# Kernel tuning notes

Hardware: AMD Instinct MI355X
Metric: run time of the kernel (lower is better)

Reference implementation:

```python
import jax, jax.numpy as jnp
import numpy as np

N_DRUGS, N_TAILS, N_RELS = 10000, 20000, 100
E = 1_000_000
DIM = 64
SAMPLE_SIZE = 16
BN_EPS = 1e-5


def _xavier(k, shp):
    lim = np.sqrt(6.0 / (shp[0] + shp[1]))
    return jax.random.uniform(k, shp, jnp.float32, -lim, lim)


def setup_inputs() -> dict:
    key = jax.random.key(0)
    ks = jax.random.split(key, 12)
    DKG = jnp.stack([
        jax.random.randint(ks[0], (E,), 0, N_DRUGS, jnp.int32),   # head drug
        jax.random.randint(ks[1], (E,), 0, N_TAILS, jnp.int32),   # tail entity
        jax.random.randint(ks[2], (E,), 0, N_RELS, jnp.int32),    # relation
    ], axis=1)
    return {
        "HFEmbeding": jax.random.normal(ks[3], (N_DRUGS, DIM), jnp.float32),
        "X": jax.random.normal(ks[4], (N_DRUGS,), jnp.float32),
        "drug_emb": _xavier(ks[5], (N_DRUGS, DIM)),
        "rel_emb": _xavier(ks[6], (N_RELS, DIM)),
        "tail_emb": _xavier(ks[7], (N_TAILS, DIM)),
        "W1": _xavier(ks[8], (DIM, DIM)), "b1": jnp.zeros((DIM,), jnp.float32),
        "W2": _xavier(ks[9], (DIM, DIM)), "b2": jnp.zeros((DIM,), jnp.float32),
        "Wc": _xavier(ks[10], (2 * DIM, DIM)), "bc": jnp.zeros((DIM,), jnp.float32),
        "gamma": jnp.ones((DIM,), jnp.float32), "beta": jnp.zeros((DIM,), jnp.float32),
        "DKG": DKG,
    }


def _sampling_plan(head):
    """Vectorized stand-in for the per-node WeightedRandomSampler loop.
    deg >= S: uniform sample of S neighbor edges WITHOUT replacement (Gumbel-style
    per-segment random ranking). deg < S: keep all edges, plus (S - deg) extra
    draws WITH replacement. Purely index-valued; independent of float params."""
    k1, k2 = jax.random.split(jax.random.key(42))
    ones = jnp.ones_like(head)
    deg = jax.ops.segment_sum(ones, head, num_segments=N_DRUGS)          # [N]
    offsets = jnp.cumsum(deg) - deg                                      # CSR row starts
    r = jax.random.uniform(k1, head.shape)
    perm = jnp.lexsort((r, head))          # sorted by head, shuffled within segment
    head_sorted = head[perm]
    rank = jnp.arange(head.shape[0]) - offsets[head_sorted]
    keep = rank < SAMPLE_SIZE              # covers both branches' base sums
    # with-replacement extras for deg < S
    u = jax.random.randint(k2, (N_DRUGS, SAMPLE_SIZE), 0, jnp.iinfo(jnp.int32).max)
    safe_deg = jnp.maximum(deg, 1)
    extra_edge = perm[offsets[:, None] + u % safe_deg[:, None]]          # [N, S]
    need = jnp.clip(SAMPLE_SIZE - deg, 0)
    extra_mask = (jnp.arange(SAMPLE_SIZE)[None, :] < need[:, None]) & (deg[:, None] > 0)
    return perm, head_sorted, keep, extra_edge, extra_mask


def reference(HFEmbeding, X, drug_emb, rel_emb, tail_emb, W1, b1, W2, b2, Wc, bc, gamma, beta, DKG):
    head, tail, rel = DKG[:, 0], DKG[:, 1], DKG[:, 2]
    # edge semantics score: MLP(sigma) over hadamard of head & relation embeddings
    h = drug_emb[head] * rel_emb[rel]                       # [E, D]
    h = jax.nn.sigmoid(h @ W1 + b1) @ W2 + b2
    score = jnp.sum(h, axis=1, keepdims=True)               # [E, 1]
    temp = score * tail_emb[tail]                           # [E, D]
    perm, head_sorted, keep, extra_edge, extra_mask = _sampling_plan(head)
    neigh = jax.ops.segment_sum(jnp.where(keep[:, None], temp[perm], 0.0),
                                head_sorted, num_segments=N_DRUGS)       # [N, D]
    neigh = neigh + jnp.sum(temp[extra_edge] * extra_mask[..., None], axis=1)
    cat = jnp.concatenate([drug_emb, neigh], axis=1)        # [N, 2D]
    y = cat @ Wc + bc
    # BatchNorm1d, training mode (batch statistics, biased variance)
    mean = jnp.mean(y, axis=0)
    var = jnp.var(y, axis=0)
    out = gamma * (y - mean) * jax.lax.rsqrt(var + BN_EPS) + beta
    return (HFEmbeding, out, X)
```

## Files before the change

### kernel.cpp

```cpp
#include <hip/hip_runtime.h>
#include <stdint.h>

#define NDRUGS 10000
#define NTAILS 20000
#define NE     1000000
#define SSIZE  16
#define NPART  192
#define CSLOT  96

typedef unsigned int  u32;
typedef unsigned short u16;
typedef unsigned long long u64;
typedef __attribute__((ext_vector_type(8))) short bf16x8;
typedef __attribute__((ext_vector_type(4))) float f32x4;
#define U64MAX 0xffffffffffffffffULL

__host__ __device__ __forceinline__ void tf2x32(u32 k0, u32 k1, u32 x0, u32 x1,
                                                u32& o0, u32& o1) {
  u32 ks2 = k0 ^ k1 ^ 0x1BD11BDAu;
  x0 += k0; x1 += k1;
#define TFR(r) { x0 += x1; x1 = (x1 << r) | (x1 >> (32 - r)); x1 ^= x0; }
  TFR(13) TFR(15) TFR(26) TFR(6)
  x0 += k1; x1 += ks2 + 1u;
  TFR(17) TFR(29) TFR(16) TFR(24)
  x0 += ks2; x1 += k0 + 2u;
  TFR(13) TFR(15) TFR(26) TFR(6)
  x0 += k0; x1 += k1 + 3u;
  TFR(17) TFR(29) TFR(16) TFR(24)
  x0 += k1; x1 += ks2 + 4u;
  TFR(13) TFR(15) TFR(26) TFR(6)
  x0 += ks2; x1 += k0 + 5u;
#undef TFR
  o0 = x0; o1 = x1;
}

__device__ __forceinline__ u32 rbits32(u32 kx, u32 ky, u32 i) {
  u32 o0, o1;
  tf2x32(kx, ky, 0u, i, o0, o1);
  return o0 ^ o1;
}
#define SELKEY(e) ((((u64)(rbits32(k1x, k1y, (u32)(e)) >> 9)) << 32) | (u32)(e))
#define CSWAP(x, y) { u64 lo_ = x < y ? x : y; u64 hi_ = x < y ? y : x; x = lo_; y = hi_; }

__device__ __forceinline__ float q16(float f) {
  u32 x = __builtin_bit_cast(u32, f);
  u32 lsb = (x >> 16) & 1u;
  x = (x + 0x7fffu + lsb) & 0xffff0000u;
  return __builtin_bit_cast(float, x);
}
__device__ __forceinline__ u16 rne16(float f) {
  u32 x = __builtin_bit_cast(u32, f);
  u32 lsb = (x >> 16) & 1u;
  return (u16)((x + 0x7fffu + lsb) >> 16);
}
__device__ __forceinline__ float bfbits2f(u16 b) {
  u32 x = ((u32)b) << 16;
  return __builtin_bit_cast(float, x);
}

__global__ __launch_bounds__(256) void k_hist(const int4* __restrict__ dkg4,
                                              u32* __restrict__ part32) {
  __shared__ int hist[NDRUGS];
  for (int j = threadIdx.x; j < NDRUGS; j += 256) hist[j] = 0;
  __syncthreads();
  for (int i = blockIdx.x * 256 + threadIdx.x; i < NE / 4; i += NPART * 256) {
    int4 A = dkg4[3 * i], B = dkg4[3 * i + 1], C = dkg4[3 * i + 2];
    atomicAdd(&hist[A.x], 1);
    atomicAdd(&hist[A.w], 1);
    atomicAdd(&hist[B.z], 1);
    atomicAdd(&hist[C.y], 1);
  }
  __syncthreads();
  u32* p = part32 + blockIdx.x * (NDRUGS / 2);
  for (int j = threadIdx.x; j < NDRUGS / 2; j += 256)
    p[j] = (u32)hist[2 * j] | ((u32)hist[2 * j + 1] << 16);
}

__global__ __launch_bounds__(256) void k_thr(const u32* __restrict__ part32,
                                             int* __restrict__ deg,
                                             u32* __restrict__ thr,
                                             int* __restrict__ cnt,
                                             int* __restrict__ nflag) {
  int t = blockIdx.x * 256 + threadIdx.x;
  if (t == 0) *nflag = 0;
  if (t >= NDRUGS / 2) return;
  int d0 = 0, d1 = 0;
  for (int b = 0; b < NPART; b++) {
    u32 v = part32[b * (NDRUGS / 2) + t];
    d0 += (int)(v & 0xffffu);
    d1 += (int)(v >> 16);
  }
  int d = 2 * t;
  deg[d] = d0;  deg[d + 1] = d1;
  cnt[d] = 0;   cnt[d + 1] = 0;
  thr[d]     = (d0 <= 40) ? 0x800000u
                          : (402653184u + (u32)d0 - 1u) / (u32)d0;
  thr[d + 1] = (d1 <= 40) ? 0x800000u
                          : (402653184u + (u32)d1 - 1u) / (u32)d1;
}

__global__ __launch_bounds__(256) void k_cand(const int4* __restrict__ dkg4,
                                              const u32* __restrict__ thr,
                                              int* __restrict__ cnt,
                                              int* __restrict__ cand,
                                              int* __restrict__ nflag,
                                              int* __restrict__ flaglist,
                                              u32 k1x, u32 k1y) {
  __shared__ u32 thr_l[NDRUGS];
  for (int j = threadIdx.x; j < NDRUGS; j += 256) thr_l[j] = thr[j];
  __syncthreads();
  int i = blockIdx.x * 256 + threadIdx.x;
  if (i >= NE / 4) return;
  int4 A = dkg4[3 * i], B = dkg4[3 * i + 1], C = dkg4[3 * i + 2];
  int h[4] = {A.x, A.w, B.z, C.y};
  int e0 = 4 * i;
#pragma unroll
  for (int k = 0; k < 4; k++) {
    u32 rb = rbits32(k1x, k1y, (u32)(e0 + k));
    if ((rb >> 9) < thr_l[h[k]]) {
      int pos = atomicAdd(&cnt[h[k]], 1);
      if (pos < CSLOT) cand[h[k] * CSLOT + pos] = e0 + k;
      else if (pos == CSLOT) {
        int ix = atomicAdd(nflag, 1);
        if (ix < 256) flaglist[ix] = h[k];
      }
    }
  }
}

__global__ __launch_bounds__(256) void k_select(const int* __restrict__ cand,
                                                const int* __restrict__ cnt,
                                                const int* __restrict__ deg,
                                                int* __restrict__ sel,
                                                int* __restrict__ nflag,
                                                int* __restrict__ flaglist,
                                                u32 k1x, u32 k1y,
                                                u32 khx, u32 khy,
                                                u32 klx, u32 kly) {
  __shared__ int asel[4][16];
  int tid = threadIdx.x, lane = tid & 63, wv = tid >> 6;
  int d = blockIdx.x * 4 + wv;
  if (d >= NDRUGS) return;
  int dg = deg[d], n = cnt[d], off = d * CSLOT;
  if (dg <= 0) {
    if (lane < 16) sel[d * SSIZE + lane] = -1;
    return;
  }
  if (dg >= SSIZE) {
    if (n < SSIZE || n > CSLOT) {
      if (lane == 0) {
        int ix = atomicAdd(nflag, 1);
        if (ix < 256) flaglist[ix] = d;
      }
      return;
    }
    u64 a0 = U64MAX, a1 = U64MAX;
    if (lane < n)      a0 = SELKEY(cand[off + lane]);
    if (lane + 64 < n) a1 = SELKEY(cand[off + lane + 64]);
    CSWAP(a0, a1)
    int h = 0; u32 my = 0;
#pragma unroll
    for (int r = 0; r < SSIZE; r++) {
      u64 ex = (h == 0) ? a0 : (h == 1) ? a1 : U64MAX;
      u64 g = ex;
#pragma unroll
      for (int m = 1; m < 64; m <<= 1) {
        u64 o = __shfl_xor(g, m, 64);
        g = o < g ? o : g;
      }
      if (lane == r) my = (u32)g;
      if (ex == g) h++;
    }
    if (lane < 16) sel[d * SSIZE + lane] = (int)my;
  } else {
    u64 a0 = (lane < n) ? SELKEY(cand[off + lane]) : U64MAX;
    int h = 0;
    for (int r = 0; r < n; r++) {
      u64 ex = (h == 0) ? a0 : U64MAX;
      u64 g = ex;
#pragma unroll
      for (int m = 1; m < 64; m <<= 1) {
        u64 o = __shfl_xor(g, m, 64);
        g = o < g ? o : g;
      }
      if (lane == 0) asel[wv][r] = (int)(u32)g;
      if (ex == g) h++;
    }
    if (lane < n) sel[d * SSIZE + lane] = asel[wv][lane];
    int need = SSIZE - n;
    const u32 span = 0x7fffffffu;
    if (lane < need) {
      u32 j = (u32)(d * SSIZE + lane);
      u32 hi = rbits32(khx, khy, j) % span;
      u32 lo = rbits32(klx, kly, j) % span;
      u32 u = (hi * 2u + lo) % span;
      int idx = (int)(u % (u32)n);
      sel[d * SSIZE + n + lane] = asel[wv][idx];
    }
  }
}

__global__ __launch_bounds__(256) void k_fix(const int* __restrict__ dkg,
                                             const int* __restrict__ nflag,
                                             const int* __restrict__ flaglist,
                                             int* __restrict__ sel,
                                             u32 k1x, u32 k1y) {
  int nf = *nflag;
  if (nf <= 0) return;
  if (nf > 256) nf = 256;
  __shared__ u64 pool[256 * 16];
  int tid = threadIdx.x;
  for (int f = 0; f < nf; f++) {
    int d = flaglist[f];
    u64 loc[16];
#pragma unroll
    for (int i = 0; i < 16; i++) loc[i] = U64MAX;
    u64 mx = U64MAX; int mi = 0;
    for (int e = tid; e < NE; e += 256) {
      if (dkg[3 * e] == d) {
        u64 k = SELKEY(e);
        if (k < mx) {
          loc[mi] = k; mx = 0;
          for (int i = 0; i < 16; i++)
            if (loc[i] > mx) { mx = loc[i]; mi = i; }
        }
      }
    }
#pragma unroll
    for (int i = 0; i < 16; i++) pool[tid * 16 + i] = loc[i];
    __syncthreads();
    if (tid == 0) {
      u64 best[16];
#pragma unroll
      for (int i = 0; i < 16; i++) best[i] = U64MAX;
      u64 bm = U64MAX; int bi = 0;
      for (int i = 0; i < 256 * 16; i++) {
        u64 k = pool[i];
        if (k < bm) {
          best[bi] = k; bm = 0;
          for (int j = 0; j < 16; j++)
            if (best[j] > bm) { bm = best[j]; bi = j; }
        }
      }
      for (int s = 0; s < 16; s++) sel[d * SSIZE + s] = (int)(u32)best[s];
    }
    __syncthreads();
  }
}

__global__ __launch_bounds__(256, 2) void k_gather(const int* __restrict__ sel,
                                                   const int* __restrict__ dkg,
                                                   const float* __restrict__ drug,
                                                   const float* __restrict__ rel,
                                                   const float* __restrict__ tail,
                                                   const float* __restrict__ W1,
                                                   const float* __restrict__ b1,
                                                   const float* __restrict__ W2,
                                                   const float* __restrict__ b2,
                                                   float* __restrict__ neigh,
                                                   float* __restrict__ psq) {
  __shared__ __align__(16) u16 Vh[4][16][72];
  __shared__ __align__(16) u16 Vl[4][16][72];
  __shared__ float rsp[4][64];
  int tid = threadIdx.x, lane = tid & 63, wv = tid >> 6;
  int quad = lane >> 4, c = lane & 15;

  if (blockIdx.x == 0 && tid < 128) psq[tid] = 0.f;
  {
    int r_ = tid & 63, ks = tid >> 6;
    float s = 0.f;
    for (int k = ks * 16; k < ks * 16 + 16; k++) s += q16(W2[r_ * 64 + k]);
    rsp[ks][r_] = s;
  }
  __syncthreads();

  bf16x8 bw[4][2];
#pragma unroll
  for (int t = 0; t < 4; t++)
#pragma unroll
    for (int s = 0; s < 2; s++) {
      union { short h[8]; bf16x8 v; } u;
#pragma unroll
      for (int jj = 0; jj < 8; jj++)
        u.h[jj] = (short)rne16(W1[(s * 32 + quad * 8 + jj) * 64 + t * 16 + c]);
      bw[t][s] = u.v;
    }
  float b1t[4], w2t[4];
#pragma unroll
  for (int t = 0; t < 4; t++) {
    b1t[t] = q16(b1[t * 16 + c]);
    int rr = t * 16 + c;
    w2t[t] = rsp[0][rr] + rsp[1][rr] + rsp[2][rr] + rsp[3][rr];
  }
  float sb2 = q16(b2[lane]);
#pragma unroll
  for (int m = 32; m; m >>= 1) sb2 += __shfl_xor(sb2, m, 64);

  int d0 = (blockIdx.x * 4 + wv) * 4;
  int sv = sel[d0 * SSIZE + lane];
  int es = sv < 0 ? 0 : sv;
  int rlv = dkg[3 * es + 2];
  int tlv = dkg[3 * es + 1];

#pragma unroll 1
  for (int dd = 0; dd < 4; dd++) {
    int d = d0 + dd;
    float dr = q16(drug[d * 64 + lane]);
#pragma unroll
    for (int e = 0; e < 16; e++) {
      int rl = __shfl(rlv, dd * 16 + e, 64);
      float v = dr * q16(rel[rl * 64 + lane]);
      u16 hb = rne16(v);
      float lo = v - bfbits2f(hb);
      Vh[wv][e][lane] = hb;
      Vl[wv][e][lane] = rne16(lo);
    }
    bf16x8 ah[2], al[2];
#pragma unroll
    for (int s = 0; s < 2; s++) {
      ah[s] = *(const bf16x8*)&Vh[wv][c][s * 32 + quad * 8];
      al[s] = *(const bf16x8*)&Vl[wv][c][s * 32 + quad * 8];
    }
    f32x4 acc[4];
#pragma unroll
    for (int t = 0; t < 4; t++) {
      acc[t] = (f32x4){b1t[t], b1t[t], b1t[t], b1t[t]};
#pragma unroll
      for (int s = 0; s < 2; s++) {
        acc[t] = __builtin_amdgcn_mfma_f32_16x16x32_bf16(ah[s], bw[t][s], acc[t], 0, 0, 0);
        acc[t] = __builtin_amdgcn_mfma_f32_16x16x32_bf16(al[s], bw[t][s], acc[t], 0, 0, 0);
      }
    }
    float p[4] = {0.f, 0.f, 0.f, 0.f};
#pragma unroll
    for (int t = 0; t < 4; t++)
#pragma unroll
      for (int r = 0; r < 4; r++)
        p[r] = fmaf(1.f / (1.f + __expf(-acc[t][r])), w2t[t], p[r]);
#pragma unroll
    for (int m = 1; m < 16; m <<= 1) {
#pragma unroll
      for (int r = 0; r < 4; r++) p[r] += __shfl_xor(p[r], m, 64);
    }
#pragma unroll
    for (int r = 0; r < 4; r++) p[r] += sb2;
    float a0 = 0.f, a1 = 0.f, a2 = 0.f, a3 = 0.f;
#pragma unroll
    for (int e = 0; e < 16; e += 4) {
#pragma unroll
      for (int k = 0; k < 4; k++) {
        int sl = dd * 16 + e + k;
        int ee = __shfl(sv, sl, 64);
        int tl = __shfl(tlv, sl, 64);
        float sc = __shfl(p[(e + k) & 3], ((e + k) >> 2) << 4, 64);
        float tv = q16(tail[tl * 64 + lane]);
        if (ee >= 0) {
          if (k == 0) a0 = fmaf(sc, tv, a0);
          else if (k == 1) a1 = fmaf(sc, tv, a1);
          else if (k == 2) a2 = fmaf(sc, tv, a2);
          else a3 = fmaf(sc, tv, a3);
        }
      }
    }
    neigh[d * 64 + lane] = (a0 + a1) + (a2 + a3);
  }
}

__global__ __launch_bounds__(256, 2) void k_epi(const float* __restrict__ drug,
                                                const float* __restrict__ neigh,
                                                const float* __restrict__ Wc,
                                                const float* __restrict__ bc,
                                                float* __restrict__ y,
                                                float* __restrict__ ps,
                                                float* __restrict__ pq) {
  __shared__ __align__(16) u16 Ah[4][16][136];
  __shared__ __align__(16) u16 Al[4][16][72];
  __shared__ float Sp[16][64], Qp[16][64];
  int tid = threadIdx.x, lane = tid & 63, wv = tid >> 6;
  int quad = lane >> 4, c = lane & 15;

  bf16x8 bw[4][4];
#pragma unroll
  for (int t = 0; t < 4; t++)
#pragma unroll
    for (int s = 0; s < 4; s++) {
      union { short h[8]; bf16x8 v; } u;
#pragma unroll
      for (int jj = 0; jj < 8; jj++)
        u.h[jj] = (short)rne16(Wc[(s * 32 + quad * 8 + jj) * 64 + t * 16 + c]);
      bw[t][s] = u.v;
    }
  float bct[4];
#pragma unroll
  for (int t = 0; t < 4; t++) bct[t] = q16(bc[t * 16 + c]);

  int D0 = (blockIdx.x * 4 + wv) * 16;
#pragma unroll 1
  for (int rr = 0; rr < 16; rr++) {
    int d = D0 + rr;
    int dsafe = d < NDRUGS ? d : NDRUGS - 1;
    float dv = q16(drug[dsafe * 64 + lane]);
    Ah[wv][rr][lane] = rne16(dv);
    float nv = neigh[dsafe * 64 + lane];
    u16 nh = rne16(nv);
    Ah[wv][rr][64 + lane] = nh;
    Al[wv][rr][lane] = rne16(nv - bfbits2f(nh));
  }
  f32x4 acc[4];
#pragma unroll
  for (int t = 0; t < 4; t++) acc[t] = (f32x4){bct[t], bct[t], bct[t], bct[t]};
#pragma unroll
  for (int s = 0; s < 4; s++) {
    bf16x8 a = *(const bf16x8*)&Ah[wv][c][s * 32 + quad * 8];
#pragma unroll
    for (int t = 0; t < 4; t++)
      acc[t] = __builtin_amdgcn_mfma_f32_16x16x32_bf16(a, bw[t][s], acc[t], 0, 0, 0);
  }
#pragma unroll
  for (int s = 0; s < 2; s++) {
    bf16x8 a = *(const bf16x8*)&Al[wv][c][s * 32 + quad * 8];
#pragma unroll
    for (int t = 0; t < 4; t++)
      acc[t] = __builtin_amdgcn_mfma_f32_16x16x32_bf16(a, bw[t][2 + s], acc[t], 0, 0, 0);
  }
#pragma unroll
  for (int t = 0; t < 4; t++) {
    float s = 0.f, q = 0.f;
#pragma unroll
    for (int r = 0; r < 4; r++) {
      int row = D0 + quad * 4 + r;
      if (row < NDRUGS) {
        float v = acc[t][r];
        y[row * 64 + t * 16 + c] = v;
        s += v;
        q = fmaf(v, v, q);
      }
    }
    Sp[wv * 4 + quad][t * 16 + c] = s;
    Qp[wv * 4 + quad][t * 16 + c] = q;
  }
  __syncthreads();
  if (tid < 64) {
    float s = 0.f, q = 0.f;
#pragma unroll
    for (int p = 0; p < 16; p++) { s += Sp[p][tid]; q += Qp[p][tid]; }
    atomicAdd(&ps[tid], s);
    atomicAdd(&pq[tid], q);
  }
}

__global__ __launch_bounds__(256) void k_final(const float4* __restrict__ HFE4,
                                               const float4* __restrict__ Xv4,
                                               const float* __restrict__ gamma,
                                               const float* __restrict__ beta,
                                               const float* __restrict__ ps,
                                               const float* __restrict__ pq,
                                               float4* __restrict__ out4) {
  int i4 = blockIdx.x * 256 + threadIdx.x;
  if (i4 < 160000) {
    float4 a = HFE4[i4];
    a.x = q16(a.x); a.y = q16(a.y); a.z = q16(a.z); a.w = q16(a.w);
    out4[i4] = a;
  } else if (i4 < 320000) {
    int idx4 = i4 - 160000;
    int j0 = (idx4 * 4) & 63;
    float4 S = *(const float4*)&ps[j0];
    float4 Q = *(const float4*)&pq[j0];
    float4 v = out4[i4];
    float4 r;
#define BN1(X, SS, QQ, JJ)                                                 \
    { float m = SS / 10000.f;                                              \
      float inv = rsqrtf(QQ / 10000.f - m * m + 1e-5f);                    \
      r.X = q16(fmaf(q16(gamma[JJ]) * (v.X - m), inv, q16(beta[JJ]))); }
    BN1(x, S.x, Q.x, j0 + 0)
    BN1(y, S.y, Q.y, j0 + 1)
    BN1(z, S.z, Q.z, j0 + 2)
    BN1(w, S.w, Q.w, j0 + 3)
#undef BN1
    out4[i4] = r;
  } else if (i4 < 322500) {
    float4 a = Xv4[i4 - 320000];
    a.x = q16(a.x); a.y = q16(a.y); a.z = q16(a.z); a.w = q16(a.w);
    out4[i4] = a;
  }
}

extern "C" void kernel_launch(void* const* d_in, const int* in_sizes, int n_in,
                              void* d_out, int out_size, void* d_ws, size_t ws_size,
                              hipStream_t stream) {
  const float* drug = (const float*)d_in[2];
  const float* rel  = (const float*)d_in[3];
  const float* tail = (const float*)d_in[4];
  const float* W1   = (const float*)d_in[5];
  const float* b1   = (const float*)d_in[6];
  const float* W2   = (const float*)d_in[7];
  const float* b2   = (const float*)d_in[8];
  const float* Wc   = (const float*)d_in[9];
  const float* bc   = (const float*)d_in[10];
  const float* gam  = (const float*)d_in[11];
  const float* bet  = (const float*)d_in[12];
  const int*   dkg  = (const int*)d_in[13];
  float* out = (float*)d_out;
  float* y = out + 640000;

  char* w = (char*)d_ws;
  u32*   part   = (u32*)(w);
  int*   cand   = (int*)(w);
  float* neigh  = (float*)(w);
  float* ps     = (float*)(w + 2600000);
  float* pq     = (float*)(w + 2600256);
  int*   flagl  = (int*)(w + 3900000);
  int*   nflag  = (int*)(w + 3904096);
  int*   sel    = (int*)(w + 4000000);
  int*   cnt    = (int*)(w + 4640000);
  u32*   thr    = (u32*)(w + 4680000);
  int*   deg    = (int*)(w + 4720000);

  u32 k1x, k1y, k2x, k2y, khx, khy, klx, kly;
  tf2x32(0u, 42u, 0u, 0u, k1x, k1y);
  tf2x32(0u, 42u, 0u, 1u, k2x, k2y);
  tf2x32(k2x, k2y, 0u, 0u, khx, khy);
  tf2x32(k2x, k2y, 0u, 1u, klx, kly);

  k_hist<<<NPART, 256, 0, stream>>>((const int4*)dkg, part);
  k_thr<<<(NDRUGS / 2 + 255) / 256, 256, 0, stream>>>(part, deg, thr, cnt, nflag);
  k_cand<<<(NE / 4 + 255) / 256, 256, 0, stream>>>((const int4*)dkg, thr, cnt,
                                                   cand, nflag, flagl, k1x, k1y);
  k_select<<<2500, 256, 0, stream>>>(cand, cnt, deg, sel, nflag, flagl,
                                     k1x, k1y, khx, khy, klx, kly);
  k_fix<<<1, 256, 0, stream>>>(dkg, nflag, flagl, sel, k1x, k1y);
  k_gather<<<625, 256, 0, stream>>>(sel, dkg, drug, rel, tail,
                                    W1, b1, W2, b2, neigh, ps);
  k_epi<<<157, 256, 0, stream>>>(drug, neigh, Wc, bc, y, ps, pq);
  k_final<<<(322500 + 255) / 256, 256, 0, stream>>>((const float4*)d_in[0],
                                                    (const float4*)d_in[1],
                                                    gam, bet, ps, pq,
                                                    (float4*)out);
}
```

Baseline: 217.4 us.

## Fuse gather and concat-linear epilogue, pad atomic counters, shard BN stats

Merges the gather kernel and the Wc projection/BatchNorm-statistics epilogue into one kernel, so the neigh intermediate no longer goes through global memory and one launch is removed. Per-drug candidate counters are padded to 64-byte strides (zeroed with a memset) to cut atomic contention and false sharing. BN sum/sumsq atomics are spread across 16 shards, which the final kernel then reduces. CSLOT shrinks from 96 to 84 to fit the new workspace layout, which may send more drugs down the slow fallback path.

```diff
diff --git a/kernel.cpp b/kernel.cpp
--- a/kernel.cpp
+++ b/kernel.cpp
@@ -6,7 +6,7 @@
 #define NE     1000000
 #define SSIZE  16
 #define NPART  192
-#define CSLOT  96
+#define CSLOT  84
 
 typedef unsigned int  u32;
 typedef unsigned short u16;
@@ -79,10 +79,12 @@
 __global__ __launch_bounds__(256) void k_thr(const u32* __restrict__ part32,
                                              int* __restrict__ deg,
                                              u32* __restrict__ thr,
-                                             int* __restrict__ cnt,
-                                             int* __restrict__ nflag) {
+                                             int* __restrict__ nflag,
+                                             float* __restrict__ ps,
+                                             float* __restrict__ pq) {
   int t = blockIdx.x * 256 + threadIdx.x;
   if (t == 0) *nflag = 0;
+  if (t < 1024) { ps[t] = 0.f; pq[t] = 0.f; }
   if (t >= NDRUGS / 2) return;
   int d0 = 0, d1 = 0;
   for (int b = 0; b < NPART; b++) {
@@ -92,7 +94,6 @@
   }
   int d = 2 * t;
   deg[d] = d0;  deg[d + 1] = d1;
-  cnt[d] = 0;   cnt[d + 1] = 0;
   thr[d]     = (d0 <= 40) ? 0x800000u
                           : (402653184u + (u32)d0 - 1u) / (u32)d0;
   thr[d + 1] = (d1 <= 40) ? 0x800000u
@@ -101,7 +102,7 @@
 
 __global__ __launch_bounds__(256) void k_cand(const int4* __restrict__ dkg4,
                                               const u32* __restrict__ thr,
-                                              int* __restrict__ cnt,
+                                              int* __restrict__ cntp,
                                               int* __restrict__ cand,
                                               int* __restrict__ nflag,
                                               int* __restrict__ flaglist,
@@ -118,7 +119,7 @@
   for (int k = 0; k < 4; k++) {
     u32 rb = rbits32(k1x, k1y, (u32)(e0 + k));
     if ((rb >> 9) < thr_l[h[k]]) {
-      int pos = atomicAdd(&cnt[h[k]], 1);
+      int pos = atomicAdd(&cntp[h[k] * 16], 1);
       if (pos < CSLOT) cand[h[k] * CSLOT + pos] = e0 + k;
       else if (pos == CSLOT) {
         int ix = atomicAdd(nflag, 1);
@@ -129,7 +130,7 @@
 }
 
 __global__ __launch_bounds__(256) void k_select(const int* __restrict__ cand,
-                                                const int* __restrict__ cnt,
+                                                const int* __restrict__ cntp,
                                                 const int* __restrict__ deg,
                                                 int* __restrict__ sel,
                                                 int* __restrict__ nflag,
@@ -141,7 +142,7 @@
   int tid = threadIdx.x, lane = tid & 63, wv = tid >> 6;
   int d = blockIdx.x * 4 + wv;
   if (d >= NDRUGS) return;
-  int dg = deg[d], n = cnt[d], off = d * CSLOT;
+  int dg = deg[d], n = cntp[d * 16], off = d * CSLOT;
   if (dg <= 0) {
     if (lane < 16) sel[d * SSIZE + lane] = -1;
     return;
@@ -248,24 +249,28 @@
   }
 }
 
-__global__ __launch_bounds__(256, 2) void k_gather(const int* __restrict__ sel,
-                                                   const int* __restrict__ dkg,
-                                                   const float* __restrict__ drug,
-                                                   const float* __restrict__ rel,
-                                                   const float* __restrict__ tail,
-                                                   const float* __restrict__ W1,
-                                                   const float* __restrict__ b1,
-                                                   const float* __restrict__ W2,
-                                                   const float* __restrict__ b2,
-                                                   float* __restrict__ neigh,
-                                                   float* __restrict__ psq) {
+__global__ __launch_bounds__(256, 2) void k_gepi(const int* __restrict__ sel,
+                                                 const int* __restrict__ dkg,
+                                                 const float* __restrict__ drug,
+                                                 const float* __restrict__ rel,
+                                                 const float* __restrict__ tail,
+                                                 const float* __restrict__ W1,
+                                                 const float* __restrict__ b1,
+                                                 const float* __restrict__ W2,
+                                                 const float* __restrict__ b2,
+                                                 const float* __restrict__ Wc,
+                                                 const float* __restrict__ bc,
+                                                 float* __restrict__ y,
+                                                 float* __restrict__ ps,
+                                                 float* __restrict__ pq) {
   __shared__ __align__(16) u16 Vh[4][16][72];
   __shared__ __align__(16) u16 Vl[4][16][72];
   __shared__ float rsp[4][64];
+  __shared__ __align__(16) u16 NAh[16][136];
+  __shared__ __align__(16) u16 NAl[16][72];
   int tid = threadIdx.x, lane = tid & 63, wv = tid >> 6;
   int quad = lane >> 4, c = lane & 15;
 
-  if (blockIdx.x == 0 && tid < 128) psq[tid] = 0.f;
   {
     int r_ = tid & 63, ks = tid >> 6;
     float s = 0.f;
@@ -362,90 +367,51 @@
         }
       }
     }
-    neigh[d * 64 + lane] = (a0 + a1) + (a2 + a3);
-  }
-}
-
-__global__ __launch_bounds__(256, 2) void k_epi(const float* __restrict__ drug,
-                                                const float* __restrict__ neigh,
-                                                const float* __restrict__ Wc,
-                                                const float* __restrict__ bc,
-                                                float* __restrict__ y,
-                                                float* __restrict__ ps,
-                                                float* __restrict__ pq) {
-  __shared__ __align__(16) u16 Ah[4][16][136];
-  __shared__ __align__(16) u16 Al[4][16][72];
-  __shared__ float Sp[16][64], Qp[16][64];
-  int tid = threadIdx.x, lane = tid & 63, wv = tid >> 6;
-  int quad = lane >> 4, c = lane & 15;
-
-  bf16x8 bw[4][4];
-#pragma unroll
-  for (int t = 0; t < 4; t++)
-#pragma unroll
-    for (int s = 0; s < 4; s++) {
-      union { short h[8]; bf16x8 v; } u;
-#pragma unroll
-      for (int jj = 0; jj < 8; jj++)
-        u.h[jj] = (short)rne16(Wc[(s * 32 + quad * 8 + jj) * 64 + t * 16 + c]);
-      bw[t][s] = u.v;
-    }
-  float bct[4];
-#pragma unroll
-  for (int t = 0; t < 4; t++) bct[t] = q16(bc[t * 16 + c]);
-
-  int D0 = (blockIdx.x * 4 + wv) * 16;
-#pragma unroll 1
-  for (int rr = 0; rr < 16; rr++) {
-    int d = D0 + rr;
-    int dsafe = d < NDRUGS ? d : NDRUGS - 1;
-    float dv = q16(drug[dsafe * 64 + lane]);
-    Ah[wv][rr][lane] = rne16(dv);
-    float nv = neigh[dsafe * 64 + lane];
+    float nv = (a0 + a1) + (a2 + a3);
+    int row = wv * 4 + dd;
+    NAh[row][lane] = rne16(dr);
     u16 nh = rne16(nv);
-    Ah[wv][rr][64 + lane] = nh;
-    Al[wv][rr][lane] = rne16(nv - bfbits2f(nh));
-  }
-  f32x4 acc[4];
-#pragma unroll
-  for (int t = 0; t < 4; t++) acc[t] = (f32x4){bct[t], bct[t], bct[t], bct[t]};
+    NAh[row][64 + lane] = nh;
+    NAl[row][lane] = rne16(nv - bfbits2f(nh));
+  }
+  __syncthreads();
+
+  bf16x8 bwc[4];
 #pragma unroll
   for (int s = 0; s < 4; s++) {
-    bf16x8 a = *(const bf16x8*)&Ah[wv][c][s * 32 + quad * 8];
-#pragma unroll
-    for (int t = 0; t < 4; t++)
-      acc[t] = __builtin_amdgcn_mfma_f32_16x16x32_bf16(a, bw[t][s], acc[t], 0, 0, 0);
+    union { short h[8]; bf16x8 v; } u;
+#pragma unroll
+    for (int jj = 0; jj < 8; jj++)
+      u.h[jj] = (short)rne16(Wc[(s * 32 + quad * 8 + jj) * 64 + wv * 16 + c]);
+    bwc[s] = u.v;
+  }
+  float bct = q16(bc[wv * 16 + c]);
+  f32x4 acc = (f32x4){bct, bct, bct, bct};
+#pragma unroll
+  for (int s = 0; s < 4; s++) {
+    bf16x8 a = *(const bf16x8*)&NAh[c][s * 32 + quad * 8];
+    acc = __builtin_amdgcn_mfma_f32_16x16x32_bf16(a, bwc[s], acc, 0, 0, 0);
   }
 #pragma unroll
   for (int s = 0; s < 2; s++) {
-    bf16x8 a = *(const bf16x8*)&Al[wv][c][s * 32 + quad * 8];
-#pragma unroll
-    for (int t = 0; t < 4; t++)
-      acc[t] = __builtin_amdgcn_mfma_f32_16x16x32_bf16(a, bw[t][2 + s], acc[t], 0, 0, 0);
-  }
-#pragma unroll
-  for (int t = 0; t < 4; t++) {
-    float s = 0.f, q = 0.f;
-#pragma unroll
-    for (int r = 0; r < 4; r++) {
-      int row = D0 + quad * 4 + r;
-      if (row < NDRUGS) {
-        float v = acc[t][r];
-        y[row * 64 + t * 16 + c] = v;
-        s += v;
-        q = fmaf(v, v, q);
-      }
-    }
-    Sp[wv * 4 + quad][t * 16 + c] = s;
-    Qp[wv * 4 + quad][t * 16 + c] = q;
-  }
-  __syncthreads();
-  if (tid < 64) {
-    float s = 0.f, q = 0.f;
-#pragma unroll
-    for (int p = 0; p < 16; p++) { s += Sp[p][tid]; q += Qp[p][tid]; }
-    atomicAdd(&ps[tid], s);
-    atomicAdd(&pq[tid], q);
+    bf16x8 a = *(const bf16x8*)&NAl[c][s * 32 + quad * 8];
+    acc = __builtin_amdgcn_mfma_f32_16x16x32_bf16(a, bwc[2 + s], acc, 0, 0, 0);
+  }
+  float ssum = 0.f, qsum = 0.f;
+#pragma unroll
+  for (int r = 0; r < 4; r++) {
+    int row = blockIdx.x * 16 + quad * 4 + r;
+    float v = acc[r];
+    y[row * 64 + wv * 16 + c] = v;
+    ssum += v;
+    qsum = fmaf(v, v, qsum);
+  }
+  ssum += __shfl_xor(ssum, 16, 64); ssum += __shfl_xor(ssum, 32, 64);
+  qsum += __shfl_xor(qsum, 16, 64); qsum += __shfl_xor(qsum, 32, 64);
+  if (quad == 0) {
+    int sh = (blockIdx.x & 15) * 64 + wv * 16 + c;
+    atomicAdd(&ps[sh], ssum);
+    atomicAdd(&pq[sh], qsum);
   }
 }
 
@@ -464,8 +430,14 @@
   } else if (i4 < 320000) {
     int idx4 = i4 - 160000;
     int j0 = (idx4 * 4) & 63;
-    float4 S = *(const float4*)&ps[j0];
-    float4 Q = *(const float4*)&pq[j0];
+    float4 S = {0.f, 0.f, 0.f, 0.f}, Q = {0.f, 0.f, 0.f, 0.f};
+#pragma unroll
+    for (int sh = 0; sh < 16; sh++) {
+      float4 a = *(const float4*)&ps[sh * 64 + j0];
+      float4 b = *(const float4*)&pq[sh * 64 + j0];
+      S.x += a.x; S.y += a.y; S.z += a.z; S.w += a.w;
+      Q.x += b.x; Q.y += b.y; Q.z += b.z; Q.w += b.w;
+    }
     float4 v = out4[i4];
     float4 r;
 #define BN1(X, SS, QQ, JJ)                                                 \
@@ -506,15 +478,14 @@
   char* w = (char*)d_ws;
   u32*   part   = (u32*)(w);
   int*   cand   = (int*)(w);
-  float* neigh  = (float*)(w);
-  float* ps     = (float*)(w + 2600000);
-  float* pq     = (float*)(w + 2600256);
-  int*   flagl  = (int*)(w + 3900000);
-  int*   nflag  = (int*)(w + 3904096);
+  int*   cntp   = (int*)(w + 3360000);
   int*   sel    = (int*)(w + 4000000);
-  int*   cnt    = (int*)(w + 4640000);
-  u32*   thr    = (u32*)(w + 4680000);
-  int*   deg    = (int*)(w + 4720000);
+  u32*   thr    = (u32*)(w + 4640000);
+  int*   deg    = (int*)(w + 4680000);
+  int*   flagl  = (int*)(w + 4720000);
+  int*   nflag  = (int*)(w + 4721024);
+  float* ps     = (float*)(w + 4721152);
+  float* pq     = (float*)(w + 4725248);
 
   u32 k1x, k1y, k2x, k2y, khx, khy, klx, kly;
   tf2x32(0u, 42u, 0u, 0u, k1x, k1y);
@@ -523,15 +494,15 @@
   tf2x32(k2x, k2y, 0u, 1u, klx, kly);
 
   k_hist<<<NPART, 256, 0, stream>>>((const int4*)dkg, part);
-  k_thr<<<(NDRUGS / 2 + 255) / 256, 256, 0, stream>>>(part, deg, thr, cnt, nflag);
-  k_cand<<<(NE / 4 + 255) / 256, 256, 0, stream>>>((const int4*)dkg, thr, cnt,
+  k_thr<<<(NDRUGS / 2 + 255) / 256, 256, 0, stream>>>(part, deg, thr, nflag, ps, pq);
+  hipMemsetAsync(cntp, 0, 16 * NDRUGS * sizeof(int), stream);
+  k_cand<<<(NE / 4 + 255) / 256, 256, 0, stream>>>((const int4*)dkg, thr, cntp,
                                                    cand, nflag, flagl, k1x, k1y);
-  k_select<<<2500, 256, 0, stream>>>(cand, cnt, deg, sel, nflag, flagl,
+  k_select<<<2500, 256, 0, stream>>>(cand, cntp, deg, sel, nflag, flagl,
                                      k1x, k1y, khx, khy, klx, kly);
   k_fix<<<1, 256, 0, stream>>>(dkg, nflag, flagl, sel, k1x, k1y);
-  k_gather<<<625, 256, 0, stream>>>(sel, dkg, drug, rel, tail,
-                                    W1, b1, W2, b2, neigh, ps);
-  k_epi<<<157, 256, 0, stream>>>(drug, neigh, Wc, bc, y, ps, pq);
+  k_gepi<<<625, 256, 0, stream>>>(sel, dkg, drug, rel, tail,
+                                  W1, b1, W2, b2, Wc, bc, y, ps, pq);
   k_final<<<(322500 + 255) / 256, 256, 0, stream>>>((const float4*)d_in[0],
                                                     (const float4*)d_in[1],
                                                     gam, bet, ps, pq,
```

New measurement: 201.2 us. 7.4% less time.
